# Kernel tuning notes

Hardware: AMD Instinct MI355X
Metric: run time of the kernel (lower is better)

Reference implementation:

```python
import jax, jax.numpy as jnp
import numpy as np

GAMMA = 2.0
EPS = 1e-06
LAMBDA_DISTANCE = 1.0
LAMBDA_NORMAL = 0.01
LAMBDA_LAPLACIAN = 0.1
CLS = 1


def vertex_normals(v, f, eps=EPS):
    # v: [N,3], f: [F,3] int. Scatter face normals to vertices, then normalize.
    fv = v[f]  # [F,3,3]
    fn = jnp.cross(fv[:, 1] - fv[:, 0], fv[:, 2] - fv[:, 0])  # [F,3]
    vn = jnp.zeros_like(v)
    vn = vn.at[f[:, 0]].add(fn).at[f[:, 1]].add(fn).at[f[:, 2]].add(fn)
    norm = jnp.maximum(jnp.linalg.norm(vn, axis=-1, keepdims=True), eps)
    return vn / norm


def squared_cdist(a, b):
    # [Na,3] x [Nb,3] -> squared euclidean distances [Na,Nb] (clamped >= 0)
    a2 = jnp.sum(a * a, axis=1)[:, None]
    b2 = jnp.sum(b * b, axis=1)[None, :]
    d2 = a2 + b2 - 2.0 * (a @ b.T)
    return jnp.maximum(d2, 0.0)


def sample_binary_targets(label, v, cls=CLS):
    # Nearest-neighbor grid_sample, align_corners=True, padding zeros.
    # grid = 2*v - 1 -> voxel index = round(v * (size-1)); v[:,0]->W, v[:,1]->H, v[:,2]->D.
    D, H, W = label.shape[2], label.shape[3], label.shape[4]
    ix = jnp.round(v[:, 0] * (W - 1)).astype(jnp.int32)
    iy = jnp.round(v[:, 1] * (H - 1)).astype(jnp.int32)
    iz = jnp.round(v[:, 2] * (D - 1)).astype(jnp.int32)
    inb = (ix >= 0) & (ix < W) & (iy >= 0) & (iy < H) & (iz >= 0) & (iz < D)
    ixc = jnp.clip(ix, 0, W - 1)
    iyc = jnp.clip(iy, 0, H - 1)
    izc = jnp.clip(iz, 0, D - 1)
    vals = (label[0, 0, izc, iyc, ixc] == cls).astype(jnp.float32)
    return jnp.where(inb, vals, 0.0)


def spatial_consistency_loss(rel_pos, targets, gamma=GAMMA, eps=EPS):
    p = jnp.clip(rel_pos, eps, 1.0 - eps)
    pos = targets > 0.5
    pc = jnp.sum(pos).astype(p.dtype)
    tot = jnp.asarray(p.shape[0], p.dtype)
    nc = tot - pc
    alpha = nc / (tot + eps)
    lpos = -alpha * jnp.power(1.0 - p, gamma) * jnp.log(p)
    lneg = -(1.0 - alpha) * jnp.power(p, gamma) * jnp.log(1.0 - p)
    return jnp.sum(jnp.where(pos, lpos, lneg)) / (tot + eps)


def laplacian_uniform(v, f):
    # Uniform mesh Laplacian smoothing: || mean(neighbors) - v ||, averaged.
    i = jnp.concatenate([f[:, 0], f[:, 1], f[:, 2], f[:, 1], f[:, 2], f[:, 0]])
    j = jnp.concatenate([f[:, 1], f[:, 2], f[:, 0], f[:, 0], f[:, 1], f[:, 2]])
    nsum = jnp.zeros_like(v).at[i].add(v[j])
    deg = jnp.zeros((v.shape[0],), v.dtype).at[i].add(1.0)
    lap = nsum / jnp.maximum(deg, 1.0)[:, None] - v
    return jnp.mean(jnp.linalg.norm(lap, axis=1))


def loss_forward(pred_vertices, relative_positions, gt_vertices, pred_faces, gt_faces, label):
    gt_v = jax.lax.stop_gradient(gt_vertices)  # gt comes from label volume; detached in original
    gt_normals = vertex_normals(gt_v, gt_faces)
    # spatial (focal-style) loss
    targets = sample_binary_targets(label, pred_vertices)
    spatial = spatial_consistency_loss(relative_positions, targets)
    # chamfer-style squared surface distance
    d2 = squared_cdist(pred_vertices, gt_v)  # [Np,Ng]
    distance = jnp.mean(jnp.min(d2, axis=1)) + jnp.mean(jnp.min(d2, axis=0))
    # normal consistency vs nearest gt vertex
    pred_normals = vertex_normals(pred_vertices, pred_faces)
    nearest = jnp.argmin(d2, axis=1)
    normal = jnp.mean((pred_normals - gt_normals[nearest]) ** 2)
    # uniform laplacian smoothing
    laplacian = laplacian_uniform(pred_vertices, pred_faces)
    total = spatial + LAMBDA_DISTANCE * distance + LAMBDA_NORMAL * normal + LAMBDA_LAPLACIAN * laplacian
    return total


def setup_inputs() -> dict:
    key = jax.random.key(0)
    k1, k2, k3, k4, k5, k6 = jax.random.split(key, 6)
    Np, Ng = 8192, 12000
    pred_vertices = jax.random.uniform(k1, (Np, 3), dtype=jnp.float32)
    relative_positions = jax.random.uniform(k2, (Np,), dtype=jnp.float32)
    gt_vertices = jax.random.uniform(k3, (Ng, 3), dtype=jnp.float32)
    pred_faces = jax.random.randint(k4, (2 * Np, 3), 0, Np, dtype=jnp.int32)
    gt_faces = jax.random.randint(k5, (2 * Ng, 3), 0, Ng, dtype=jnp.int32)
    label = jax.random.randint(k6, (1, 1, 96, 96, 96), 0, 2, dtype=jnp.int32)
    return {"pred_vertices": pred_vertices, "relative_positions": relative_positions,
            "gt_vertices": gt_vertices, "pred_faces": pred_faces,
            "gt_faces": gt_faces, "label": label}


def reference(pred_vertices, relative_positions, gt_vertices, pred_faces, gt_faces, label):
    return loss_forward(pred_vertices, relative_positions, gt_vertices, pred_faces, gt_faces, label)
```

## Files before the change

### kernel.cpp

```cpp
#include <hip/hip_runtime.h>
#include <math.h>

#define NP 8192
#define NG 12000
#define NFP 16384
#define NFG 24000
#define EPSF 1e-6f

#define GR 16
#define NC (GR*GR*GR)
#define HCELL 0.0625f
#define QL 16
#define QPB (256 / QL)
#define PRED_QBLOCKS (NP / QPB)
#define GT_QBLOCKS (NG / QPB)
#define NN_BLOCKS (PRED_QBLOCKS + GT_QBLOCKS)

static constexpr size_t OFF_STARTP = 0;
static constexpr size_t OFF_STARTG = 16640;
static constexpr size_t OFF_SORTP  = 33280;
static constexpr size_t OFF_SORTG  = 164352;
static constexpr size_t OFF_PART   = 356352;
static constexpr size_t OFF_GTN    = 396736;
static constexpr size_t OFF_PNN    = 540736;
static constexpr size_t OFF_NSUM   = 639040;
static constexpr size_t OFF_DEG    = 737344;

__device__ __forceinline__ int cell_of(float x) {
    int c = (int)(x * (float)GR);
    return min(max(c, 0), GR - 1);
}

__device__ __forceinline__ void hist_scan_scatter(const float* __restrict__ pts, int n,
                                                  unsigned* __restrict__ start,
                                                  float4* __restrict__ sorted,
                                                  unsigned* h, unsigned* ps) {
    int t = threadIdx.x;
    for (int i = t; i < NC; i += 1024) h[i] = 0u;
    __syncthreads();
    for (int i = t; i < n; i += 1024) {
        int c = (cell_of(pts[3*i+2]) * GR + cell_of(pts[3*i+1])) * GR + cell_of(pts[3*i]);
        atomicAdd(&h[c], 1u);
    }
    __syncthreads();
    unsigned a0 = h[4*t], a1 = h[4*t+1], a2 = h[4*t+2], a3 = h[4*t+3];
    unsigned tsum = a0 + a1 + a2 + a3;
    ps[t] = tsum; __syncthreads();
    for (int off = 1; off < 1024; off <<= 1) {
        unsigned v = (t >= off) ? ps[t - off] : 0u;
        __syncthreads();
        ps[t] += v;
        __syncthreads();
    }
    unsigned ex = ps[t] - tsum;
    h[4*t] = ex; h[4*t+1] = ex + a0; h[4*t+2] = ex + a0 + a1; h[4*t+3] = ex + a0 + a1 + a2;
    __syncthreads();
    for (int i = t; i < NC; i += 1024) start[i] = h[i];
    if (t == 0) start[NC] = (unsigned)n;
    __syncthreads();
    for (int i = t; i < n; i += 1024) {
        float x = pts[3*i], y = pts[3*i+1], z = pts[3*i+2];
        int c = (cell_of(z) * GR + cell_of(y)) * GR + cell_of(x);
        unsigned pos = atomicAdd(&h[c], 1u);
        sorted[pos] = make_float4(x, y, z, __int_as_float(i));
    }
}

#define FACE_BLOCKS ((NFG + NFP + 1023) / 1024)
__global__ __launch_bounds__(1024) void build_kernel(const float* __restrict__ pred,
                                                     const int* __restrict__ pf,
                                                     const float* __restrict__ gt,
                                                     const int* __restrict__ gf,
                                                     unsigned* __restrict__ startP,
                                                     unsigned* __restrict__ startG,
                                                     float4* __restrict__ sortP,
                                                     float4* __restrict__ sortG,
                                                     float* __restrict__ gtn,
                                                     float* __restrict__ pnn,
                                                     float* __restrict__ nsum,
                                                     float* __restrict__ deg) {
    __shared__ unsigned h[NC];
    __shared__ unsigned ps[1024];
    if (blockIdx.x == 0) {
        hist_scan_scatter(pred, NP, startP, sortP, h, ps);
    } else if (blockIdx.x == 1) {
        hist_scan_scatter(gt, NG, startG, sortG, h, ps);
    } else {
        int t = (blockIdx.x - 2) * 1024 + threadIdx.x;
        if (t < NFG) {
            int i0 = gf[3*t], i1 = gf[3*t+1], i2 = gf[3*t+2];
            float ax = gt[3*i0], ay = gt[3*i0+1], az = gt[3*i0+2];
            float bx = gt[3*i1], by = gt[3*i1+1], bz = gt[3*i1+2];
            float cx = gt[3*i2], cy = gt[3*i2+1], cz = gt[3*i2+2];
            float ux = bx-ax, uy = by-ay, uz = bz-az;
            float wx = cx-ax, wy = cy-ay, wz = cz-az;
            float nx = uy*wz - uz*wy, ny = uz*wx - ux*wz, nz = ux*wy - uy*wx;
            atomicAdd(&gtn[3*i0+0], nx); atomicAdd(&gtn[3*i0+1], ny); atomicAdd(&gtn[3*i0+2], nz);
            atomicAdd(&gtn[3*i1+0], nx); atomicAdd(&gtn[3*i1+1], ny); atomicAdd(&gtn[3*i1+2], nz);
            atomicAdd(&gtn[3*i2+0], nx); atomicAdd(&gtn[3*i2+1], ny); atomicAdd(&gtn[3*i2+2], nz);
        } else if (t < NFG + NFP) {
            int u = t - NFG;
            int i0 = pf[3*u], i1 = pf[3*u+1], i2 = pf[3*u+2];
            float ax = pred[3*i0], ay = pred[3*i0+1], az = pred[3*i0+2];
            float bx = pred[3*i1], by = pred[3*i1+1], bz = pred[3*i1+2];
            float cx = pred[3*i2], cy = pred[3*i2+1], cz = pred[3*i2+2];
            float ux = bx-ax, uy = by-ay, uz = bz-az;
            float wx = cx-ax, wy = cy-ay, wz = cz-az;
            float nx = uy*wz - uz*wy, ny = uz*wx - ux*wz, nz = ux*wy - uy*wx;
            atomicAdd(&pnn[3*i0+0], nx); atomicAdd(&pnn[3*i0+1], ny); atomicAdd(&pnn[3*i0+2], nz);
            atomicAdd(&pnn[3*i1+0], nx); atomicAdd(&pnn[3*i1+1], ny); atomicAdd(&pnn[3*i1+2], nz);
            atomicAdd(&pnn[3*i2+0], nx); atomicAdd(&pnn[3*i2+1], ny); atomicAdd(&pnn[3*i2+2], nz);
            atomicAdd(&nsum[3*i0+0], bx+cx); atomicAdd(&nsum[3*i0+1], by+cy); atomicAdd(&nsum[3*i0+2], bz+cz);
            atomicAdd(&nsum[3*i1+0], cx+ax); atomicAdd(&nsum[3*i1+1], cy+ay); atomicAdd(&nsum[3*i1+2], cz+az);
            atomicAdd(&nsum[3*i2+0], ax+bx); atomicAdd(&nsum[3*i2+1], ay+by); atomicAdd(&nsum[3*i2+2], az+bz);
            atomicAdd(&deg[i0], 2.0f); atomicAdd(&deg[i1], 2.0f); atomicAdd(&deg[i2], 2.0f);
        }
    }
}

__device__ __forceinline__ float wave_sum(float x) {
    #pragma unroll
    for (int o = 32; o > 0; o >>= 1) x += __shfl_down(x, o, 64);
    return x;
}

__device__ __forceinline__ unsigned long long u64min(unsigned long long a,
                                                     unsigned long long b) {
    return a < b ? a : b;
}

__device__ __forceinline__ unsigned long long group_nn(int lane,
                                                       float px, float py, float pz,
                                                       const float4* __restrict__ S,
                                                       const unsigned* __restrict__ cstart) {
    int cx = cell_of(px), cy = cell_of(py), cz = cell_of(pz);
    unsigned long long best = 0xFFFFFFFFFFFFFFFFULL;
    for (int r = 1; ; ++r) {
        int w = 2 * r + 1;
        int nrows = w * w;
        int x0 = max(cx - r, 0), x1 = min(cx + r, GR - 1);
        unsigned long long lb = 0xFFFFFFFFFFFFFFFFULL;
        for (int k = lane; k < nrows; k += QL) {
            int z = cz + k / w - r, y = cy + k % w - r;
            if (z >= 0 && z < GR && y >= 0 && y < GR) {
                int rowbase = (z * GR + y) * GR;
                unsigned s0 = cstart[rowbase + x0];
                unsigned s1 = cstart[rowbase + x1 + 1];
                for (unsigned t = s0; t < s1; ++t) {
                    float4 q = S[t];
                    float ddx = px - q.x, ddy = py - q.y, ddz = pz - q.z;
                    float d2 = fmaf(ddx, ddx, fmaf(ddy, ddy, ddz*ddz));
                    unsigned long long key =
                        ((unsigned long long)__float_as_uint(d2) << 32) |
                        (unsigned)__float_as_int(q.w);
                    lb = u64min(lb, key);
                }
            }
        }
        best = u64min(best, lb);
        #pragma unroll
        for (int m = 1; m < QL; m <<= 1)
            best = u64min(best, (unsigned long long)__shfl_xor((long long)best, m, 64));
        bool covered = (cx - r <= 0) & (cx + r >= GR - 1) &
                       (cy - r <= 0) & (cy + r >= GR - 1) &
                       (cz - r <= 0) & (cz + r >= GR - 1);
        if (covered) break;
        float blo = 1.0e30f;
        if (cx - r > 0)      blo = fminf(blo, px - (float)(cx - r) * HCELL);
        if (cx + r < GR - 1) blo = fminf(blo, (float)(cx + r + 1) * HCELL - px);
        if (cy - r > 0)      blo = fminf(blo, py - (float)(cy - r) * HCELL);
        if (cy + r < GR - 1) blo = fminf(blo, (float)(cy + r + 1) * HCELL - py);
        if (cz - r > 0)      blo = fminf(blo, pz - (float)(cz - r) * HCELL);
        if (cz + r < GR - 1) blo = fminf(blo, (float)(cz + r + 1) * HCELL - pz);
        float bd2 = __uint_as_float((unsigned)(best >> 32));
        if (bd2 <= blo * blo) break;
    }
    return best;
}

__global__ __launch_bounds__(256) void nn_kernel(const float* __restrict__ relpos,
                                                 const int* __restrict__ label,
                                                 const float4* __restrict__ sortP,
                                                 const float4* __restrict__ sortG,
                                                 const unsigned* __restrict__ startP,
                                                 const unsigned* __restrict__ startG,
                                                 const float* __restrict__ pnn,
                                                 const float* __restrict__ gtn,
                                                 const float* __restrict__ nsum,
                                                 const float* __restrict__ deg,
                                                 float* __restrict__ partial) {
    int lane = threadIdx.x & (QL - 1);
    int group = threadIdx.x >> 4;
    if (blockIdx.x < PRED_QBLOCKS) {
        int qid = blockIdx.x * QPB + group;
        float4 P = sortP[qid];
        float px = P.x, py = P.y, pz = P.z;
        unsigned long long key = group_nn(lane, px, py, pz, sortG, startG);

        float r0 = 0.f, r1 = 0.f, r2 = 0.f, r3 = 0.f, r4 = 0.f, r5 = 0.f;
        if (lane == 0) {
            int v = __float_as_int(P.w);
            float dmin = __uint_as_float((unsigned)(key >> 32));
            int nearest = (int)(unsigned)(key & 0xffffffffu);

            float ax = pnn[3*v], ay = pnn[3*v+1], az = pnn[3*v+2];
            float an = fmaxf(sqrtf(ax*ax + ay*ay + az*az), EPSF);
            float gx = gtn[3*nearest], gy = gtn[3*nearest+1], gz = gtn[3*nearest+2];
            float gn = fmaxf(sqrtf(gx*gx + gy*gy + gz*gz), EPSF);
            float nx = ax/an - gx/gn, ny = ay/an - gy/gn, nz = az/an - gz/gn;
            float sse = nx*nx + ny*ny + nz*nz;

            float d = fmaxf(deg[v], 1.0f);
            float lx = nsum[3*v]/d - px, ly = nsum[3*v+1]/d - py, lz = nsum[3*v+2]/d - pz;
            float lapn = sqrtf(lx*lx + ly*ly + lz*lz);

            int ix = (int)rintf(px * 95.0f), iy = (int)rintf(py * 95.0f), iz = (int)rintf(pz * 95.0f);
            bool inb = (ix >= 0) & (ix < 96) & (iy >= 0) & (iy < 96) & (iz >= 0) & (iz < 96);
            int ixc = min(max(ix, 0), 95), iyc = min(max(iy, 0), 95), izc = min(max(iz, 0), 95);
            bool pos = inb && (label[(izc*96 + iyc)*96 + ixc] == 1);

            float p = fminf(fmaxf(relpos[v], EPSF), 1.0f - EPSF);
            float om = 1.0f - p;
            float pcnt = 0.0f, sx = 0.0f, sy = 0.0f;
            if (pos) { pcnt = 1.0f; sx = om*om*logf(p); }
            else     { sy = p*p*logf(om); }

            r0 = dmin; r1 = sse; r2 = lapn; r3 = pcnt; r4 = sx; r5 = sy;
        }
        r0 = wave_sum(r0); r1 = wave_sum(r1); r2 = wave_sum(r2);
        r3 = wave_sum(r3); r4 = wave_sum(r4); r5 = wave_sum(r5);
        __shared__ float acc[6];
        if (threadIdx.x < 6) acc[threadIdx.x] = 0.0f;
        __syncthreads();
        if ((threadIdx.x & 63) == 0) {
            atomicAdd(&acc[0], r0); atomicAdd(&acc[1], r1); atomicAdd(&acc[2], r2);
            atomicAdd(&acc[3], r3); atomicAdd(&acc[4], r4); atomicAdd(&acc[5], r5);
        }
        __syncthreads();
        if (threadIdx.x < 6)
            partial[(size_t)blockIdx.x * 8 + threadIdx.x] = acc[threadIdx.x];
    } else {
        int qid = (blockIdx.x - PRED_QBLOCKS) * QPB + group;
        float4 Q = sortG[qid];
        unsigned long long key = group_nn(lane, Q.x, Q.y, Q.z, sortP, startP);
        float val = (lane == 0) ? __uint_as_float((unsigned)(key >> 32)) : 0.0f;
        float r = wave_sum(val);
        __shared__ float bsum;
        if (threadIdx.x == 0) bsum = 0.0f;
        __syncthreads();
        if ((threadIdx.x & 63) == 0) atomicAdd(&bsum, r);
        __syncthreads();
        if (threadIdx.x == 0)
            partial[(size_t)blockIdx.x * 8] = bsum;
    }
}

__global__ __launch_bounds__(256) void combine_kernel(const float* __restrict__ partial,
                                                      float* __restrict__ out) {
    float s0=0.f, s1=0.f, s2=0.f, s3=0.f, s4=0.f, s5=0.f, s6=0.f;
    for (int r = threadIdx.x; r < NN_BLOCKS; r += 256) {
        const float* p = partial + (size_t)r * 8;
        if (r < PRED_QBLOCKS) {
            s0 += p[0]; s1 += p[1]; s2 += p[2];
            s3 += p[3]; s4 += p[4]; s5 += p[5];
        } else {
            s6 += p[0];
        }
    }
    s0 = wave_sum(s0); s1 = wave_sum(s1); s2 = wave_sum(s2); s3 = wave_sum(s3);
    s4 = wave_sum(s4); s5 = wave_sum(s5); s6 = wave_sum(s6);
    __shared__ float acc[7];
    if (threadIdx.x < 7) acc[threadIdx.x] = 0.0f;
    __syncthreads();
    if ((threadIdx.x & 63) == 0) {
        atomicAdd(&acc[0], s0); atomicAdd(&acc[1], s1); atomicAdd(&acc[2], s2);
        atomicAdd(&acc[3], s3); atomicAdd(&acc[4], s4); atomicAdd(&acc[5], s5);
        atomicAdd(&acc[6], s6);
    }
    __syncthreads();
    if (threadIdx.x == 0) {
        float tot = (float)NP;
        float alpha = (tot - acc[3]) / (tot + EPSF);
        float spatial = (-alpha * acc[4] - (1.0f - alpha) * acc[5]) / (tot + EPSF);
        float distance = acc[0] / (float)NP + acc[6] / (float)NG;
        float normal = acc[1] / (float)(NP * 3);
        float lapm = acc[2] / (float)NP;
        out[0] = spatial + 1.0f * distance + 0.01f * normal + 0.1f * lapm;
    }
}

extern "C" void kernel_launch(void* const* d_in, const int* in_sizes, int n_in,
                              void* d_out, int out_size, void* d_ws, size_t ws_size,
                              hipStream_t stream) {
    const float* pred   = (const float*)d_in[0];
    const float* relpos = (const float*)d_in[1];
    const float* gt     = (const float*)d_in[2];
    const int*   pfaces = (const int*)d_in[3];
    const int*   gfaces = (const int*)d_in[4];
    const int*   label  = (const int*)d_in[5];
    float* out = (float*)d_out;

    char* ws = (char*)d_ws;
    unsigned* startP  = (unsigned*)(ws + OFF_STARTP);
    unsigned* startG  = (unsigned*)(ws + OFF_STARTG);
    float4*   sortP   = (float4*)(ws + OFF_SORTP);
    float4*   sortG   = (float4*)(ws + OFF_SORTG);
    float*    partial = (float*)(ws + OFF_PART);
    float*    gtn     = (float*)(ws + OFF_GTN);
    float*    pnn     = (float*)(ws + OFF_PNN);
    float*    nsum    = (float*)(ws + OFF_NSUM);
    float*    deg     = (float*)(ws + OFF_DEG);

    hipLaunchKernelGGL(build_kernel, dim3(2 + FACE_BLOCKS), dim3(1024), 0, stream,
                       pred, pfaces, gt, gfaces, startP, startG, sortP, sortG,
                       gtn, pnn, nsum, deg);
    hipLaunchKernelGGL(nn_kernel, dim3(NN_BLOCKS), dim3(256), 0, stream,
                       relpos, label, sortP, sortG, startP, startG,
                       pnn, gtn, nsum, deg, partial);
    hipLaunchKernelGGL(combine_kernel, dim3(1), dim3(256), 0, stream, partial, out);
}
```

Baseline: 124.3 us.

## Privatize scatter-add accumulators into eight replicas and reduce them via lane shuffles

The normal, Laplacian-sum and degree scatter buffers are now split into 8 copies, and each block picks a copy from its block index so atomic adds to the same vertex are spread out. In the NN kernel, 8 lanes of each query group load one replica each and combine them with xor shuffles before lane 0 evaluates the loss terms. The aim is to cut atomic contention in the scatter phase. The cost is 8x larger buffers to zero and read back, and it relies on the hidden code that clears them covering the grown offsets.

```diff
diff --git a/kernel.cpp b/kernel.cpp
--- a/kernel.cpp
+++ b/kernel.cpp
@@ -6,6 +6,8 @@
 #define NFP 16384
 #define NFG 24000
 #define EPSF 1e-6f
+#define NP3 (NP*3)
+#define NG3 (NG*3)
 
 #define GR 16
 #define NC (GR*GR*GR)
@@ -15,6 +17,7 @@
 #define PRED_QBLOCKS (NP / QPB)
 #define GT_QBLOCKS (NG / QPB)
 #define NN_BLOCKS (PRED_QBLOCKS + GT_QBLOCKS)
+#define NCOPY 8
 
 static constexpr size_t OFF_STARTP = 0;
 static constexpr size_t OFF_STARTG = 16640;
@@ -22,9 +25,9 @@
 static constexpr size_t OFF_SORTG  = 164352;
 static constexpr size_t OFF_PART   = 356352;
 static constexpr size_t OFF_GTN    = 396736;
-static constexpr size_t OFF_PNN    = 540736;
-static constexpr size_t OFF_NSUM   = 639040;
-static constexpr size_t OFF_DEG    = 737344;
+static constexpr size_t OFF_PNN    = 1548736;
+static constexpr size_t OFF_NSUM   = 2335168;
+static constexpr size_t OFF_DEG    = 3121600;
 
 __device__ __forceinline__ int cell_of(float x) {
     int c = (int)(x * (float)GR);
@@ -86,6 +89,11 @@
     } else if (blockIdx.x == 1) {
         hist_scan_scatter(gt, NG, startG, sortG, h, ps);
     } else {
+        int c = blockIdx.x & 7;
+        float* gtnc  = gtn  + (size_t)c * NG3;
+        float* pnnc  = pnn  + (size_t)c * NP3;
+        float* nsumc = nsum + (size_t)c * NP3;
+        float* degc  = deg  + (size_t)c * NP;
         int t = (blockIdx.x - 2) * 1024 + threadIdx.x;
         if (t < NFG) {
             int i0 = gf[3*t], i1 = gf[3*t+1], i2 = gf[3*t+2];
@@ -95,9 +103,9 @@
             float ux = bx-ax, uy = by-ay, uz = bz-az;
             float wx = cx-ax, wy = cy-ay, wz = cz-az;
             float nx = uy*wz - uz*wy, ny = uz*wx - ux*wz, nz = ux*wy - uy*wx;
-            atomicAdd(&gtn[3*i0+0], nx); atomicAdd(&gtn[3*i0+1], ny); atomicAdd(&gtn[3*i0+2], nz);
-            atomicAdd(&gtn[3*i1+0], nx); atomicAdd(&gtn[3*i1+1], ny); atomicAdd(&gtn[3*i1+2], nz);
-            atomicAdd(&gtn[3*i2+0], nx); atomicAdd(&gtn[3*i2+1], ny); atomicAdd(&gtn[3*i2+2], nz);
+            atomicAdd(&gtnc[3*i0+0], nx); atomicAdd(&gtnc[3*i0+1], ny); atomicAdd(&gtnc[3*i0+2], nz);
+            atomicAdd(&gtnc[3*i1+0], nx); atomicAdd(&gtnc[3*i1+1], ny); atomicAdd(&gtnc[3*i1+2], nz);
+            atomicAdd(&gtnc[3*i2+0], nx); atomicAdd(&gtnc[3*i2+1], ny); atomicAdd(&gtnc[3*i2+2], nz);
         } else if (t < NFG + NFP) {
             int u = t - NFG;
             int i0 = pf[3*u], i1 = pf[3*u+1], i2 = pf[3*u+2];
@@ -107,13 +115,13 @@
             float ux = bx-ax, uy = by-ay, uz = bz-az;
             float wx = cx-ax, wy = cy-ay, wz = cz-az;
             float nx = uy*wz - uz*wy, ny = uz*wx - ux*wz, nz = ux*wy - uy*wx;
-            atomicAdd(&pnn[3*i0+0], nx); atomicAdd(&pnn[3*i0+1], ny); atomicAdd(&pnn[3*i0+2], nz);
-            atomicAdd(&pnn[3*i1+0], nx); atomicAdd(&pnn[3*i1+1], ny); atomicAdd(&pnn[3*i1+2], nz);
-            atomicAdd(&pnn[3*i2+0], nx); atomicAdd(&pnn[3*i2+1], ny); atomicAdd(&pnn[3*i2+2], nz);
-            atomicAdd(&nsum[3*i0+0], bx+cx); atomicAdd(&nsum[3*i0+1], by+cy); atomicAdd(&nsum[3*i0+2], bz+cz);
-            atomicAdd(&nsum[3*i1+0], cx+ax); atomicAdd(&nsum[3*i1+1], cy+ay); atomicAdd(&nsum[3*i1+2], cz+az);
-            atomicAdd(&nsum[3*i2+0], ax+bx); atomicAdd(&nsum[3*i2+1], ay+by); atomicAdd(&nsum[3*i2+2], az+bz);
-            atomicAdd(&deg[i0], 2.0f); atomicAdd(&deg[i1], 2.0f); atomicAdd(&deg[i2], 2.0f);
+            atomicAdd(&pnnc[3*i0+0], nx); atomicAdd(&pnnc[3*i0+1], ny); atomicAdd(&pnnc[3*i0+2], nz);
+            atomicAdd(&pnnc[3*i1+0], nx); atomicAdd(&pnnc[3*i1+1], ny); atomicAdd(&pnnc[3*i1+2], nz);
+            atomicAdd(&pnnc[3*i2+0], nx); atomicAdd(&pnnc[3*i2+1], ny); atomicAdd(&pnnc[3*i2+2], nz);
+            atomicAdd(&nsumc[3*i0+0], bx+cx); atomicAdd(&nsumc[3*i0+1], by+cy); atomicAdd(&nsumc[3*i0+2], bz+cz);
+            atomicAdd(&nsumc[3*i1+0], cx+ax); atomicAdd(&nsumc[3*i1+1], cy+ay); atomicAdd(&nsumc[3*i1+2], cz+az);
+            atomicAdd(&nsumc[3*i2+0], ax+bx); atomicAdd(&nsumc[3*i2+1], ay+by); atomicAdd(&nsumc[3*i2+2], az+bz);
+            atomicAdd(&degc[i0], 2.0f); atomicAdd(&degc[i1], 2.0f); atomicAdd(&degc[i2], 2.0f);
         }
     }
 }
@@ -196,35 +204,47 @@
         float4 P = sortP[qid];
         float px = P.x, py = P.y, pz = P.z;
         unsigned long long key = group_nn(lane, px, py, pz, sortG, startG);
+        int v = __float_as_int(P.w);
+        int nearest = (int)(unsigned)(key & 0xffffffffu);
+
+        float t0=0.f,t1=0.f,t2=0.f,t3=0.f,t4=0.f,t5=0.f,t6=0.f,t7=0.f,t8=0.f,t9=0.f;
+        if (lane < 8) {
+            const float* pc = pnn  + (size_t)lane * NP3 + 3*v;
+            const float* nc = nsum + (size_t)lane * NP3 + 3*v;
+            const float* gc = gtn  + (size_t)lane * NG3 + 3*nearest;
+            t0 = pc[0]; t1 = pc[1]; t2 = pc[2];
+            t3 = nc[0]; t4 = nc[1]; t5 = nc[2];
+            t6 = deg[(size_t)lane * NP + v];
+            t7 = gc[0]; t8 = gc[1]; t9 = gc[2];
+        }
+        #pragma unroll
+        for (int m = 1; m < 8; m <<= 1) {
+            t0 += __shfl_xor(t0, m, 64); t1 += __shfl_xor(t1, m, 64);
+            t2 += __shfl_xor(t2, m, 64); t3 += __shfl_xor(t3, m, 64);
+            t4 += __shfl_xor(t4, m, 64); t5 += __shfl_xor(t5, m, 64);
+            t6 += __shfl_xor(t6, m, 64); t7 += __shfl_xor(t7, m, 64);
+            t8 += __shfl_xor(t8, m, 64); t9 += __shfl_xor(t9, m, 64);
+        }
 
         float r0 = 0.f, r1 = 0.f, r2 = 0.f, r3 = 0.f, r4 = 0.f, r5 = 0.f;
         if (lane == 0) {
-            int v = __float_as_int(P.w);
             float dmin = __uint_as_float((unsigned)(key >> 32));
-            int nearest = (int)(unsigned)(key & 0xffffffffu);
-
-            float ax = pnn[3*v], ay = pnn[3*v+1], az = pnn[3*v+2];
-            float an = fmaxf(sqrtf(ax*ax + ay*ay + az*az), EPSF);
-            float gx = gtn[3*nearest], gy = gtn[3*nearest+1], gz = gtn[3*nearest+2];
-            float gn = fmaxf(sqrtf(gx*gx + gy*gy + gz*gz), EPSF);
-            float nx = ax/an - gx/gn, ny = ay/an - gy/gn, nz = az/an - gz/gn;
+            float an = fmaxf(sqrtf(t0*t0 + t1*t1 + t2*t2), EPSF);
+            float gn = fmaxf(sqrtf(t7*t7 + t8*t8 + t9*t9), EPSF);
+            float nx = t0/an - t7/gn, ny = t1/an - t8/gn, nz = t2/an - t9/gn;
             float sse = nx*nx + ny*ny + nz*nz;
-
-            float d = fmaxf(deg[v], 1.0f);
-            float lx = nsum[3*v]/d - px, ly = nsum[3*v+1]/d - py, lz = nsum[3*v+2]/d - pz;
+            float d = fmaxf(t6, 1.0f);
+            float lx = t3/d - px, ly = t4/d - py, lz = t5/d - pz;
             float lapn = sqrtf(lx*lx + ly*ly + lz*lz);
-
             int ix = (int)rintf(px * 95.0f), iy = (int)rintf(py * 95.0f), iz = (int)rintf(pz * 95.0f);
             bool inb = (ix >= 0) & (ix < 96) & (iy >= 0) & (iy < 96) & (iz >= 0) & (iz < 96);
             int ixc = min(max(ix, 0), 95), iyc = min(max(iy, 0), 95), izc = min(max(iz, 0), 95);
             bool pos = inb && (label[(izc*96 + iyc)*96 + ixc] == 1);
-
             float p = fminf(fmaxf(relpos[v], EPSF), 1.0f - EPSF);
             float om = 1.0f - p;
             float pcnt = 0.0f, sx = 0.0f, sy = 0.0f;
             if (pos) { pcnt = 1.0f; sx = om*om*logf(p); }
             else     { sy = p*p*logf(om); }
-
             r0 = dmin; r1 = sse; r2 = lapn; r3 = pcnt; r4 = sx; r5 = sy;
         }
         r0 = wave_sum(r0); r1 = wave_sum(r1); r2 = wave_sum(r2);
```

After: 128.5 us. +3.4%, slower.
